# Kernel optimization log

Hardware: AMD Instinct MI355X
Metric: run time of the kernel (lower is better)

Reference implementation:

```python
import jax, jax.numpy as jnp
import numpy as np

B, T, C = 2, 2048, 2048
H = 16
D = C // H  # head_dim = 128


def setup_inputs() -> dict:
    key = jax.random.key(0)
    ks = jax.random.split(key, 7)
    scale = C ** -0.5
    x = jax.random.normal(ks[0], (B, T, C), dtype=jnp.float32)
    padding_mask = jax.random.randint(ks[1], (B, T), 0, 2, dtype=jnp.int32)
    Wq = jax.random.normal(ks[2], (C, C), dtype=jnp.float32) * scale
    Wk = jax.random.normal(ks[3], (C, C), dtype=jnp.float32) * scale
    Wv = jax.random.normal(ks[4], (C, C), dtype=jnp.float32) * scale
    Wp = jax.random.normal(ks[5], (C, C), dtype=jnp.float32) * scale
    bp = jax.random.normal(ks[6], (C,), dtype=jnp.float32) * 0.01
    return {"x": x, "padding_mask": padding_mask, "Wq": Wq, "Wk": Wk,
            "Wv": Wv, "Wp": Wp, "bp": bp}


def reference(x, padding_mask, Wq, Wk, Wv, Wp, bp):
    b, t, c = x.shape
    # projections (nn.Linear: x @ W.T), split heads -> [B,H,T,D]
    q = (x @ Wq.T).reshape(b, t, H, D).transpose(0, 2, 1, 3)
    k = (x @ Wk.T).reshape(b, t, H, D).transpose(0, 2, 1, 3)
    v = (x @ Wv.T).reshape(b, t, H, D).transpose(0, 2, 1, 3)
    scores = jnp.einsum('bhtd,bhsd->bhts', q, k) * (D ** -0.5)  # [B,H,T,T]
    # padding mask broadcasts along query rows: pm[b,i] masks row i (as in torch source)
    scores = jnp.where(padding_mask[:, None, :, None] == 0, jnp.float32(-1e9), scores)
    # causal mask
    causal = jnp.tril(jnp.ones((t, t), dtype=bool))
    scores = jnp.where(causal, scores, -jnp.inf)
    attn = jax.nn.softmax(scores, axis=-1)
    ctx = jnp.einsum('bhts,bhsd->bhtd', attn, v)
    ctx = ctx.transpose(0, 2, 1, 3).reshape(b, t, c)
    return ctx @ Wp.T + bp
```

## Files before the change

### kernel.cpp

```cpp
#include <hip/hip_runtime.h>
#include <stdint.h>

typedef __attribute__((ext_vector_type(8))) short vshort8;
typedef __attribute__((ext_vector_type(4))) short vshort4;
typedef __attribute__((ext_vector_type(4))) float vfloat4;

__device__ __forceinline__ short f2bf(float f) {
  union { float f; uint32_t u; } v; v.f = f;
  uint32_t r = (v.u + 0x7FFFu + ((v.u >> 16) & 1u)) >> 16;
  return (short)r;
}
__device__ __forceinline__ void gl_lds16(const void* g, void* l) {
  __builtin_amdgcn_global_load_lds(
      (const __attribute__((address_space(1))) void*)g,
      (__attribute__((address_space(3))) void*)l, 16, 0, 0);
}

__global__ void cvt_kernel(const float* __restrict__ src, short* __restrict__ dst,
                           int n) {
  int i = (blockIdx.x * blockDim.x + threadIdx.x) * 8;
  if (i >= n) return;
  vfloat4 a = *(const vfloat4*)(src + i);
  vfloat4 b = *(const vfloat4*)(src + i + 4);
  vshort8 o;
#pragma unroll
  for (int j = 0; j < 4; ++j) { o[j] = f2bf(a[j]); o[j + 4] = f2bf(b[j]); }
  *(vshort8*)(dst + i) = o;
}

__global__ void cvt3_kernel(const float* __restrict__ s0, const float* __restrict__ s1,
                            const float* __restrict__ s2, short* __restrict__ dst, int n) {
  const float* s = (blockIdx.y == 0) ? s0 : ((blockIdx.y == 1) ? s1 : s2);
  int i = (blockIdx.x * blockDim.x + threadIdx.x) * 8;
  if (i >= n) return;
  vfloat4 a = *(const vfloat4*)(s + i);
  vfloat4 b = *(const vfloat4*)(s + i + 4);
  vshort8 o;
#pragma unroll
  for (int j = 0; j < 4; ++j) { o[j] = f2bf(a[j]); o[j + 4] = f2bf(b[j]); }
  *(vshort8*)(dst + (size_t)blockIdx.y * n + i) = o;
}

#define GEMM_MAIN_LOOP()                                                        \
  const int tid  = threadIdx.x;                                                 \
  const int lane = tid & 63;                                                    \
  const int w    = tid >> 6;                                                    \
  const int wr   = w >> 2;                                                      \
  const int wc   = w & 3;                                                       \
  const int lrow = lane & 15;                                                   \
  const int quad = lane >> 4;                                                   \
  const int swz  = lrow & 7;                                                    \
  const int m0   = blockIdx.y * 128;                                            \
  const int n0   = blockIdx.x * 256;                                            \
  const int rr   = tid >> 3;                                                    \
  const int cg8  = ((tid & 7) ^ ((tid >> 3) & 7)) * 8;                          \
  const short* Ag = Aptr + (size_t)(m0 + rr) * K + cg8;                         \
  const short* Bg = Bptr + (size_t)(n0 + rr) * K + cg8;                         \
  auto stageA = [&](int bb, int kt, int i) {                                    \
    gl_lds16(Ag + (size_t)i * 64 * K + (size_t)kt * 64,                         \
             (void*)&lds[bb][i * 4096 + tid * 8]);                              \
  };                                                                            \
  auto stageB = [&](int bb, int kt, int i) {                                    \
    gl_lds16(Bg + (size_t)i * 64 * K + (size_t)kt * 64,                         \
             (void*)&lds[bb][8192 + i * 4096 + tid * 8]);                       \
  };                                                                            \
  const int aoff = (wr * 64 + lrow) * 64;                                       \
  const int boff = (wc * 64 + lrow) * 64;                                       \
  const int g8a0 = (quad ^ swz) * 8;                                            \
  const int g8a1 = ((4 + quad) ^ swz) * 8;                                      \
  vfloat4 acc[4][4] = {};                                                       \
  const int NT = K >> 6;                                                        \
                        \
  stageA(0, 0, 0); stageA(0, 0, 1);                                             \
  stageB(0, 0, 0); stageB(0, 0, 1); stageB(0, 0, 2); stageB(0, 0, 3);           \
  stageA(1, 1, 0); stageA(1, 1, 1);                                             \
  stageB(1, 1, 0); stageB(1, 1, 1); stageB(1, 1, 2); stageB(1, 1, 3);           \
  int cbuf = 0;                                                                 \
  for (int t = 0; t < NT; ++t) {                                                \
    const short* As = lds[cbuf];                                                \
    const short* Bs = lds[cbuf] + 8192;                                         \
    const int sb = (cbuf == 0) ? 2 : cbuf - 1;            \
            \
    if (t + 1 < NT) {                                                           \
      asm volatile("s_waitcnt vmcnt(6)" ::: "memory");                          \
    } else {                                                                    \
      asm volatile("s_waitcnt vmcnt(0)" ::: "memory");                          \
    }                                                                           \
    __builtin_amdgcn_s_barrier();                                               \
    __builtin_amdgcn_sched_barrier(0);                                          \
         \
    if (t + 2 < NT) {                                                           \
      stageA(sb, t + 2, 0); stageA(sb, t + 2, 1);                               \
      stageB(sb, t + 2, 0); stageB(sb, t + 2, 1);                               \
      stageB(sb, t + 2, 2); stageB(sb, t + 2, 3);                               \
    }                                                                           \
      \
    vshort8 a[4][2], b[4][2];                                                   \
    _Pragma("unroll") for (int i = 0; i < 4; ++i) {                             \
      a[i][0] = *(const vshort8*)(As + aoff + i * 1024 + g8a0);                 \
      a[i][1] = *(const vshort8*)(As + aoff + i * 1024 + g8a1);                 \
      b[i][0] = *(const vshort8*)(Bs + boff + i * 1024 + g8a0);                 \
      b[i][1] = *(const vshort8*)(Bs + boff + i * 1024 + g8a1);                 \
    }                                                                           \
    __builtin_amdgcn_s_setprio(1);                                              \
    _Pragma("unroll") for (int mi = 0; mi < 4; ++mi)                            \
      _Pragma("unroll") for (int ni = 0; ni < 4; ++ni)                          \
        _Pragma("unroll") for (int ks = 0; ks < 2; ++ks)                        \
          acc[mi][ni] = __builtin_amdgcn_mfma_f32_16x16x32_bf16(                \
              a[mi][ks], b[ni][ks], acc[mi][ni], 0, 0, 0);                      \
    __builtin_amdgcn_s_setprio(0);                                              \
    __builtin_amdgcn_sched_barrier(0);                                          \
    cbuf = (cbuf == 2) ? 0 : cbuf + 1;                                          \
  }

__global__ __launch_bounds__(512, 2) void gemm_qkv(
    const short* __restrict__ Aptr, const short* __restrict__ Bptr,
    short* __restrict__ Qw, short* __restrict__ Kw, short* __restrict__ Vtw,
    int M, int K, float scale) {
  __shared__ __attribute__((aligned(16))) short lds[3][24576];
  GEMM_MAIN_LOOP()

  const int region = n0 >> 11;
#pragma unroll
  for (int mi = 0; mi < 4; ++mi) {
    int mbase = m0 + wr * 64 + mi * 16 + quad * 4;
#pragma unroll
    for (int ni = 0; ni < 4; ++ni) {
      int ng = n0 + wc * 64 + ni * 16 + lrow;
      int nn = ng & 2047;
      if (region == 2) {
        vshort4 sv;
#pragma unroll
        for (int r = 0; r < 4; ++r) sv[r] = f2bf(acc[mi][ni][r]);
        *(vshort4*)(Vtw + (size_t)nn * 4096 + mbase) = sv;
      } else if (region == 0) {
#pragma unroll
        for (int r = 0; r < 4; ++r)
          Qw[(size_t)(mbase + r) * 2048 + nn] = f2bf(acc[mi][ni][r] * scale);
      } else {
#pragma unroll
        for (int r = 0; r < 4; ++r)
          Kw[(size_t)(mbase + r) * 2048 + nn] = f2bf(acc[mi][ni][r]);
      }
    }
  }
}

__global__ __launch_bounds__(512, 2) void gemm_proj(
    const short* __restrict__ Aptr, const short* __restrict__ Bptr,
    float* __restrict__ C, const float* __restrict__ bias,
    int M, int K, int ldC) {
  __shared__ __attribute__((aligned(16))) short lds[3][24576];
  GEMM_MAIN_LOOP()

#pragma unroll
  for (int mi = 0; mi < 4; ++mi) {
    int mbase = m0 + wr * 64 + mi * 16 + quad * 4;
#pragma unroll
    for (int ni = 0; ni < 4; ++ni) {
      int n = n0 + wc * 64 + ni * 16 + lrow;
      float badd = bias[n];
#pragma unroll
      for (int r = 0; r < 4; ++r)
        C[(size_t)(mbase + r) * ldC + n] = acc[mi][ni][r] + badd;
    }
  }
}

__global__ __launch_bounds__(256) void attn_kernel(
    const short* __restrict__ Q, const short* __restrict__ Kg,
    const short* __restrict__ Vt, const int* __restrict__ pm,
    short* __restrict__ ctx) {
  const int T = 2048, Cd = 2048, D = 128, MT = 4096;
  __shared__ __attribute__((aligned(16))) short Ks[64][136];
  __shared__ __attribute__((aligned(16))) short Vs[144][72];
  __shared__ __attribute__((aligned(16))) short Ps[4][16][72];

  const int tid  = threadIdx.x;
  const int lane = tid & 63;
  const int w    = tid >> 6;
  const int lrow = lane & 15;
  const int quad = lane >> 4;
  const int p = blockIdx.x, h = blockIdx.y, b = blockIdx.z;

  for (int i = tid; i < 16 * 72; i += 256) {
    int rr = i / 72, cc = i % 72;
    Vs[128 + rr][cc] = (rr == 0) ? (short)0x3F80 : (short)0;
  }

#pragma unroll 1
  for (int tt = 0; tt < 2; ++tt) {
    const int qt = tt ? (31 - p) : p;
    const int q0 = qt * 64;
    const int qrow = q0 + w * 16 + quad * 4;

    vshort8 qf[4];
#pragma unroll
    for (int ks = 0; ks < 4; ++ks)
      qf[ks] = *(const vshort8*)(Q + (size_t)(b * T + q0 + w * 16 + lrow) * Cd +
                                 h * D + ks * 32 + quad * 8);
    bool keep[4];
#pragma unroll
    for (int r = 0; r < 4; ++r) keep[r] = pm[b * T + qrow + r] != 0;

    vfloat4 oacc[8] = {};
    vfloat4 osum = {};

    __syncthreads();
#pragma unroll
    for (int i = 0; i < 4; ++i) {
      int c = tid + i * 256;
      int kr = c >> 4, kc = c & 15;
      *(vfloat4*)(&Ks[kr][kc * 8]) =
          *(const vfloat4*)(Kg + (size_t)(b * T + kr) * Cd + h * D + kc * 8);
      int vr = c >> 3, vc = c & 7;
      *(vfloat4*)(&Vs[vr][vc * 8]) =
          *(const vfloat4*)(Vt + (size_t)(h * D + vr) * MT + b * T + vc * 8);
    }
    __syncthreads();

#pragma unroll 1
    for (int j = 0; j <= qt; ++j) {
      const int jn = (j < qt) ? (j + 1) : qt;
      vfloat4 pk[4], pv[4];
#pragma unroll
      for (int i = 0; i < 4; ++i) {
        int c = tid + i * 256;
        int kr = c >> 4, kc = c & 15;
        pk[i] = *(const vfloat4*)(Kg + (size_t)(b * T + jn * 64 + kr) * Cd + h * D + kc * 8);
        int vr = c >> 3, vc = c & 7;
        pv[i] = *(const vfloat4*)(Vt + (size_t)(h * D + vr) * MT + b * T + jn * 64 + vc * 8);
      }

      vfloat4 sacc[4] = {};
#pragma unroll
      for (int nt = 0; nt < 4; ++nt)
#pragma unroll
        for (int ks = 0; ks < 4; ++ks) {
          vshort8 kf = *(const vshort8*)(&Ks[nt * 16 + lrow][ks * 32 + quad * 8]);
          sacc[nt] = __builtin_amdgcn_mfma_f32_16x16x32_bf16(qf[ks], kf, sacc[nt], 0, 0, 0);
        }

#pragma unroll
      for (int nt = 0; nt < 4; ++nt) {
        int s_idx = j * 64 + nt * 16 + lrow;
#pragma unroll
        for (int r = 0; r < 4; ++r) {
          float sv = keep[r] ? sacc[nt][r] : 0.0f;
          float pe = __expf(sv - 12.0f);
          pe = (s_idx <= qrow + r) ? pe : 0.0f;
          Ps[w][quad * 4 + r][nt * 16 + lrow] = f2bf(pe);
        }
      }

      vshort8 pf[2];
#pragma unroll
      for (int kp = 0; kp < 2; ++kp)
        pf[kp] = *(const vshort8*)(&Ps[w][lrow][kp * 32 + quad * 8]);
#pragma unroll
      for (int dt = 0; dt < 8; ++dt)
#pragma unroll
        for (int kp = 0; kp < 2; ++kp) {
          vshort8 vf = *(const vshort8*)(&Vs[dt * 16 + lrow][kp * 32 + quad * 8]);
          oacc[dt] = __builtin_amdgcn_mfma_f32_16x16x32_bf16(pf[kp], vf, oacc[dt], 0, 0, 0);
        }
#pragma unroll
      for (int kp = 0; kp < 2; ++kp) {
        vshort8 vf = *(const vshort8*)(&Vs[128 + lrow][kp * 32 + quad * 8]);
        osum = __builtin_amdgcn_mfma_f32_16x16x32_bf16(pf[kp], vf, osum, 0, 0, 0);
      }

      __syncthreads();
#pragma unroll
      for (int i = 0; i < 4; ++i) {
        int c = tid + i * 256;
        int kr = c >> 4, kc = c & 15;
        *(vfloat4*)(&Ks[kr][kc * 8]) = pk[i];
        int vr = c >> 3, vc = c & 7;
        *(vfloat4*)(&Vs[vr][vc * 8]) = pv[i];
      }
      __syncthreads();
    }

    float l[4];
#pragma unroll
    for (int r = 0; r < 4; ++r)
      l[r] = fmaxf(__shfl(osum[r], (lane & 48), 64), 1e-30f);

#pragma unroll
    for (int dt = 0; dt < 8; ++dt) {
      int d = dt * 16 + lrow;
#pragma unroll
      for (int r = 0; r < 4; ++r) {
        float o = oacc[dt][r] / l[r];
        ctx[(size_t)(b * T + qrow + r) * Cd + h * D + d] = f2bf(o);
      }
    }
  }
}

extern "C" void kernel_launch(void* const* d_in, const int* in_sizes, int n_in,
                              void* d_out, int out_size, void* d_ws, size_t ws_size,
                              hipStream_t stream) {
  (void)in_sizes; (void)n_in; (void)out_size; (void)ws_size;
  const float* x  = (const float*)d_in[0];
  const int*   pm = (const int*)d_in[1];
  const float* Wq = (const float*)d_in[2];
  const float* Wk = (const float*)d_in[3];
  const float* Wv = (const float*)d_in[4];
  const float* Wp = (const float*)d_in[5];
  const float* bp = (const float*)d_in[6];
  float* out = (float*)d_out;

  const int Bb = 2, T = 2048, Cd = 2048, M = Bb * T;
  const size_t SZ = (size_t)M * Cd;
  const size_t WZ = (size_t)Cd * Cd;
  short* xb   = (short*)d_ws;
  short* Qw   = xb + SZ;
  short* Kw   = Qw + SZ;
  short* Vtw  = Kw + SZ;
  short* Cx   = Vtw + SZ;
  short* wcat = Cx + SZ;

  const int CB = 256;
  dim3 gx(((int)SZ / 8 + CB - 1) / CB);
  dim3 gw(((int)WZ / 8 + CB - 1) / CB);
  const float scale = 0.08838834764831845f;

  cvt_kernel<<<gx, CB, 0, stream>>>(x, xb, (int)SZ);
  cvt3_kernel<<<dim3(gw.x, 3), CB, 0, stream>>>(Wq, Wk, Wv, wcat, (int)WZ);

  gemm_qkv<<<dim3(6144 / 256, M / 128), 512, 0, stream>>>(
      xb, wcat, Qw, Kw, Vtw, M, Cd, scale);

  attn_kernel<<<dim3(16, 16, Bb), 256, 0, stream>>>(Qw, Kw, Vtw, pm, Cx);

  cvt_kernel<<<gw, CB, 0, stream>>>(Wp, wcat, (int)WZ);
  gemm_proj<<<dim3(Cd / 256, M / 128), 512, 0, stream>>>(Cx, wcat, out, bp, M, Cd, Cd);
}
```

Before: 373.1 us.

## Restructure attention to load K/V fragments directly from global memory

After: 512.5 us. +37.4%, slower.

```diff
diff --git a/kernel.cpp b/kernel.cpp
--- a/kernel.cpp
+++ b/kernel.cpp
@@ -70,7 +70,6 @@
   const int g8a1 = ((4 + quad) ^ swz) * 8;                                      \
   vfloat4 acc[4][4] = {};                                                       \
   const int NT = K >> 6;                                                        \
-                        \
   stageA(0, 0, 0); stageA(0, 0, 1);                                             \
   stageB(0, 0, 0); stageB(0, 0, 1); stageB(0, 0, 2); stageB(0, 0, 3);           \
   stageA(1, 1, 0); stageA(1, 1, 1);                                             \
@@ -80,7 +79,6 @@
     const short* As = lds[cbuf];                                                \
     const short* Bs = lds[cbuf] + 8192;                                         \
     const int sb = (cbuf == 0) ? 2 : cbuf - 1;            \
-            \
     if (t + 1 < NT) {                                                           \
       asm volatile("s_waitcnt vmcnt(6)" ::: "memory");                          \
     } else {                                                                    \
@@ -88,13 +86,11 @@
     }                                                                           \
     __builtin_amdgcn_s_barrier();                                               \
     __builtin_amdgcn_sched_barrier(0);                                          \
-         \
     if (t + 2 < NT) {                                                           \
       stageA(sb, t + 2, 0); stageA(sb, t + 2, 1);                               \
       stageB(sb, t + 2, 0); stageB(sb, t + 2, 1);                               \
       stageB(sb, t + 2, 2); stageB(sb, t + 2, 3);                               \
     }                                                                           \
-      \
     vshort8 a[4][2], b[4][2];                                                   \
     _Pragma("unroll") for (int i = 0; i < 4; ++i) {                             \
       a[i][0] = *(const vshort8*)(As + aoff + i * 1024 + g8a0);                 \
@@ -167,133 +163,119 @@
   }
 }
 
-__global__ __launch_bounds__(256) void attn_kernel(
+__global__ __launch_bounds__(128) void attn_kernel(
     const short* __restrict__ Q, const short* __restrict__ Kg,
     const short* __restrict__ Vt, const int* __restrict__ pm,
     short* __restrict__ ctx) {
   const int T = 2048, Cd = 2048, D = 128, MT = 4096;
-  __shared__ __attribute__((aligned(16))) short Ks[64][136];
-  __shared__ __attribute__((aligned(16))) short Vs[144][72];
-  __shared__ __attribute__((aligned(16))) short Ps[4][16][72];
+  __shared__ __attribute__((aligned(16))) short Ps[2][32][72];
 
   const int tid  = threadIdx.x;
   const int lane = tid & 63;
   const int w    = tid >> 6;
   const int lrow = lane & 15;
   const int quad = lane >> 4;
-  const int p = blockIdx.x, h = blockIdx.y, b = blockIdx.z;
-
-  for (int i = tid; i < 16 * 72; i += 256) {
-    int rr = i / 72, cc = i % 72;
-    Vs[128 + rr][cc] = (rr == 0) ? (short)0x3F80 : (short)0;
-  }
+  const int bx = blockIdx.x, h = blockIdx.y, b = blockIdx.z;
+  const int q0 = bx * 64 + w * 32;
+
+  vshort8 qf[2][4];
+#pragma unroll
+  for (int mi = 0; mi < 2; ++mi)
+#pragma unroll
+    for (int ks = 0; ks < 4; ++ks)
+      qf[mi][ks] = *(const vshort8*)(Q + (size_t)(b * T + q0 + mi * 16 + lrow) * Cd +
+                                     h * D + ks * 32 + quad * 8);
+  bool keep[2][4];
+#pragma unroll
+  for (int mi = 0; mi < 2; ++mi)
+#pragma unroll
+    for (int r = 0; r < 4; ++r)
+      keep[mi][r] = pm[b * T + q0 + mi * 16 + quad * 4 + r] != 0;
+
+  vfloat4 oacc[2][8] = {};
+  vfloat4 osum[2] = {};
+  vshort8 ones;
+#pragma unroll
+  for (int i = 0; i < 8; ++i) ones[i] = (short)0x3F80;
 
 #pragma unroll 1
-  for (int tt = 0; tt < 2; ++tt) {
-    const int qt = tt ? (31 - p) : p;
-    const int q0 = qt * 64;
-    const int qrow = q0 + w * 16 + quad * 4;
-
-    vshort8 qf[4];
-#pragma unroll
-    for (int ks = 0; ks < 4; ++ks)
-      qf[ks] = *(const vshort8*)(Q + (size_t)(b * T + q0 + w * 16 + lrow) * Cd +
-                                 h * D + ks * 32 + quad * 8);
-    bool keep[4];
-#pragma unroll
-    for (int r = 0; r < 4; ++r) keep[r] = pm[b * T + qrow + r] != 0;
-
-    vfloat4 oacc[8] = {};
-    vfloat4 osum = {};
-
-    __syncthreads();
-#pragma unroll
-    for (int i = 0; i < 4; ++i) {
-      int c = tid + i * 256;
-      int kr = c >> 4, kc = c & 15;
-      *(vfloat4*)(&Ks[kr][kc * 8]) =
-          *(const vfloat4*)(Kg + (size_t)(b * T + kr) * Cd + h * D + kc * 8);
-      int vr = c >> 3, vc = c & 7;
-      *(vfloat4*)(&Vs[vr][vc * 8]) =
-          *(const vfloat4*)(Vt + (size_t)(h * D + vr) * MT + b * T + vc * 8);
-    }
-    __syncthreads();
-
-#pragma unroll 1
-    for (int j = 0; j <= qt; ++j) {
-      const int jn = (j < qt) ? (j + 1) : qt;
-      vfloat4 pk[4], pv[4];
-#pragma unroll
-      for (int i = 0; i < 4; ++i) {
-        int c = tid + i * 256;
-        int kr = c >> 4, kc = c & 15;
-        pk[i] = *(const vfloat4*)(Kg + (size_t)(b * T + jn * 64 + kr) * Cd + h * D + kc * 8);
-        int vr = c >> 3, vc = c & 7;
-        pv[i] = *(const vfloat4*)(Vt + (size_t)(h * D + vr) * MT + b * T + jn * 64 + vc * 8);
-      }
-
-      vfloat4 sacc[4] = {};
+  for (int j = 0; j <= bx; ++j) {
+    const short* Kb = Kg + (size_t)(b * T + j * 64) * Cd + h * D;
+
+    vshort8 kf[4][4];
+#pragma unroll
+    for (int nt = 0; nt < 4; ++nt)
+#pragma unroll
+      for (int ks = 0; ks < 4; ++ks)
+        kf[nt][ks] = *(const vshort8*)(Kb + (size_t)(nt * 16 + lrow) * Cd +
+                                       ks * 32 + quad * 8);
+
+    vfloat4 sacc[2][4] = {};
+#pragma unroll
+    for (int mi = 0; mi < 2; ++mi)
 #pragma unroll
       for (int nt = 0; nt < 4; ++nt)
 #pragma unroll
-        for (int ks = 0; ks < 4; ++ks) {
-          vshort8 kf = *(const vshort8*)(&Ks[nt * 16 + lrow][ks * 32 + quad * 8]);
-          sacc[nt] = __builtin_amdgcn_mfma_f32_16x16x32_bf16(qf[ks], kf, sacc[nt], 0, 0, 0);
-        }
-
+        for (int ks = 0; ks < 4; ++ks)
+          sacc[mi][nt] = __builtin_amdgcn_mfma_f32_16x16x32_bf16(
+              qf[mi][ks], kf[nt][ks], sacc[mi][nt], 0, 0, 0);
+
+    vshort8 vf[8][2];
+#pragma unroll
+    for (int dt = 0; dt < 8; ++dt)
+#pragma unroll
+      for (int kp = 0; kp < 2; ++kp)
+        vf[dt][kp] = *(const vshort8*)(Vt + (size_t)(h * D + dt * 16 + lrow) * MT +
+                                       b * T + j * 64 + kp * 32 + quad * 8);
+
+#pragma unroll
+    for (int mi = 0; mi < 2; ++mi)
 #pragma unroll
       for (int nt = 0; nt < 4; ++nt) {
         int s_idx = j * 64 + nt * 16 + lrow;
 #pragma unroll
         for (int r = 0; r < 4; ++r) {
-          float sv = keep[r] ? sacc[nt][r] : 0.0f;
+          int qr = q0 + mi * 16 + quad * 4 + r;
+          float sv = keep[mi][r] ? sacc[mi][nt][r] : 0.0f;
           float pe = __expf(sv - 12.0f);
-          pe = (s_idx <= qrow + r) ? pe : 0.0f;
-          Ps[w][quad * 4 + r][nt * 16 + lrow] = f2bf(pe);
+          pe = (s_idx <= qr) ? pe : 0.0f;
+          Ps[w][mi * 16 + quad * 4 + r][nt * 16 + lrow] = f2bf(pe);
         }
       }
 
-      vshort8 pf[2];
+    vshort8 pf[2][2];
+#pragma unroll
+    for (int mi = 0; mi < 2; ++mi)
 #pragma unroll
       for (int kp = 0; kp < 2; ++kp)
-        pf[kp] = *(const vshort8*)(&Ps[w][lrow][kp * 32 + quad * 8]);
+        pf[mi][kp] = *(const vshort8*)(&Ps[w][mi * 16 + lrow][kp * 32 + quad * 8]);
+
+#pragma unroll
+    for (int mi = 0; mi < 2; ++mi) {
+#pragma unroll
+      for (int kp = 0; kp < 2; ++kp)
+        osum[mi] = __builtin_amdgcn_mfma_f32_16x16x32_bf16(pf[mi][kp], ones, osum[mi], 0, 0, 0);
 #pragma unroll
       for (int dt = 0; dt < 8; ++dt)
 #pragma unroll
-        for (int kp = 0; kp < 2; ++kp) {
-          vshort8 vf = *(const vshort8*)(&Vs[dt * 16 + lrow][kp * 32 + quad * 8]);
-          oacc[dt] = __builtin_amdgcn_mfma_f32_16x16x32_bf16(pf[kp], vf, oacc[dt], 0, 0, 0);
-        }
-#pragma unroll
-      for (int kp = 0; kp < 2; ++kp) {
-        vshort8 vf = *(const vshort8*)(&Vs[128 + lrow][kp * 32 + quad * 8]);
-        osum = __builtin_amdgcn_mfma_f32_16x16x32_bf16(pf[kp], vf, osum, 0, 0, 0);
-      }
-
-      __syncthreads();
-#pragma unroll
-      for (int i = 0; i < 4; ++i) {
-        int c = tid + i * 256;
-        int kr = c >> 4, kc = c & 15;
-        *(vfloat4*)(&Ks[kr][kc * 8]) = pk[i];
-        int vr = c >> 3, vc = c & 7;
-        *(vfloat4*)(&Vs[vr][vc * 8]) = pv[i];
-      }
-      __syncthreads();
+        for (int kp = 0; kp < 2; ++kp)
+          oacc[mi][dt] = __builtin_amdgcn_mfma_f32_16x16x32_bf16(
+              pf[mi][kp], vf[dt][kp], oacc[mi][dt], 0, 0, 0);
     }
-
+  }
+
+#pragma unroll
+  for (int mi = 0; mi < 2; ++mi) {
     float l[4];
 #pragma unroll
-    for (int r = 0; r < 4; ++r)
-      l[r] = fmaxf(__shfl(osum[r], (lane & 48), 64), 1e-30f);
-
+    for (int r = 0; r < 4; ++r) l[r] = fmaxf(osum[mi][r], 1e-30f);
 #pragma unroll
     for (int dt = 0; dt < 8; ++dt) {
       int d = dt * 16 + lrow;
 #pragma unroll
       for (int r = 0; r < 4; ++r) {
-        float o = oacc[dt][r] / l[r];
-        ctx[(size_t)(b * T + qrow + r) * Cd + h * D + d] = f2bf(o);
+        float o = oacc[mi][dt][r] / l[r];
+        ctx[(size_t)(b * T + q0 + mi * 16 + quad * 4 + r) * Cd + h * D + d] = f2bf(o);
       }
     }
   }
@@ -333,7 +315,7 @@
   gemm_qkv<<<dim3(6144 / 256, M / 128), 512, 0, stream>>>(
       xb, wcat, Qw, Kw, Vtw, M, Cd, scale);
 
-  attn_kernel<<<dim3(16, 16, Bb), 256, 0, stream>>>(Qw, Kw, Vtw, pm, Cx);
+  attn_kernel<<<dim3(32, 16, Bb), 128, 0, stream>>>(Qw, Kw, Vtw, pm, Cx);
 
   cvt_kernel<<<gw, CB, 0, stream>>>(Wp, wcat, (int)WZ);
   gemm_proj<<<dim3(Cd / 256, M / 128), 512, 0, stream>>>(Cx, wcat, out, bp, M, Cd, Cd);
```
